# Kernel tuning notes

Hardware: AMD Instinct MI355X
Metric: run time of the kernel (lower is better)

## Reference

```python
import jax, jax.numpy as jnp
import numpy as np

B, T, C, F = 2, 2048, 2048, 8192
LN_EPS = 1e-5


def setup_inputs() -> dict:
    key = jax.random.key(0)
    ks = jax.random.split(key, 24)
    rn = lambda k, s, sc=1.0: jax.random.normal(k, s, jnp.float32) * sc
    un = lambda k, s: jax.random.uniform(k, s, jnp.float32)
    inp = {}
    inp['x'] = rn(ks[0], (B, T, C))
    inp['att_shift'] = rn(ks[1], (B, C))
    # wkv_state rows: aa (num), bb (den), pp (running max exponent)
    inp['wkv_state'] = jnp.stack([jnp.zeros((B, C)), jnp.zeros((B, C)),
                                  jnp.full((B, C), -1e38)], axis=1)
    inp['ffn_shift'] = rn(ks[2], (B, C))
    inp['ln1_g'] = jnp.ones(C); inp['ln1_b'] = jnp.zeros(C)
    inp['ln2_g'] = jnp.ones(C); inp['ln2_b'] = jnp.zeros(C)
    inp['tmk'] = un(ks[3], (C,)); inp['tmv'] = un(ks[4], (C,)); inp['tmr'] = un(ks[5], (C,))
    inp['time_decay'] = rn(ks[6], (C,), 0.5)
    inp['time_first'] = rn(ks[7], (C,), 0.5)
    inp['Wk'] = rn(ks[8], (C, C), 0.02); inp['Wv'] = rn(ks[9], (C, C), 0.02)
    inp['Wr'] = rn(ks[10], (C, C), 0.02); inp['Wo'] = rn(ks[11], (C, C), 0.02)
    inp['fmk'] = un(ks[12], (C,)); inp['fmr'] = un(ks[13], (C,))
    inp['Fk'] = rn(ks[14], (C, F), 0.02)
    inp['Fr'] = rn(ks[15], (C, C), 0.02)
    inp['Fv'] = rn(ks[16], (F, C), 0.02)
    return inp


def layer_norm(x, g, b):
    m = jnp.mean(x, axis=-1, keepdims=True)
    v = jnp.mean(jnp.square(x - m), axis=-1, keepdims=True)
    return (x - m) * jax.lax.rsqrt(v + LN_EPS) * g + b


def wkv(w, u, k, v, state):
    # w: -exp(time_decay) [C], u: time_first [C]; k,v: [B,T,C]; state: [B,3,C]
    def step(carry, kv_t):
        aa, bb, pp = carry
        kt, vt = kv_t
        ww = u + kt
        p = jnp.maximum(pp, ww)
        e1 = jnp.exp(pp - p)
        e2 = jnp.exp(ww - p)
        y = (e1 * aa + e2 * vt) / (e1 * bb + e2)
        ww2 = pp + w
        p2 = jnp.maximum(ww2, kt)
        e1b = jnp.exp(ww2 - p2)
        e2b = jnp.exp(kt - p2)
        return (e1b * aa + e2b * vt, e1b * bb + e2b, p2), y
    carry0 = (state[:, 0], state[:, 1], state[:, 2])
    (aa, bb, pp), ys = jax.lax.scan(step, carry0,
                                    (k.transpose(1, 0, 2), v.transpose(1, 0, 2)))
    return ys.transpose(1, 0, 2), jnp.stack([aa, bb, pp], axis=1)


def reference(x, att_shift, wkv_state, ffn_shift, ln1_g, ln1_b, ln2_g, ln2_b,
              tmk, tmv, tmr, time_decay, time_first, Wk, Wv, Wr, Wo,
              fmk, fmr, Fk, Fr, Fv):
    # ---- time-mix (attention) ----
    x1 = layer_norm(x, ln1_g, ln1_b)
    xx = jnp.concatenate([att_shift[:, None, :], x1[:, :-1]], axis=1)
    xk = x1 * tmk + xx * (1.0 - tmk)
    xv = x1 * tmv + xx * (1.0 - tmv)
    xr = x1 * tmr + xx * (1.0 - tmr)
    k = jnp.einsum('btc,cd->btd', xk, Wk)
    v = jnp.einsum('btc,cd->btd', xv, Wv)
    r = jnp.einsum('btc,cd->btd', xr, Wr)
    y, new_wkv = wkv(-jnp.exp(time_decay), time_first, k, v, wkv_state)
    x = x + jnp.einsum('btd,dc->btc', jax.nn.sigmoid(r) * y, Wo)
    # ---- channel-mix (FFN) ----
    x2 = layer_norm(x, ln2_g, ln2_b)
    xx2 = jnp.concatenate([ffn_shift[:, None, :], x2[:, :-1]], axis=1)
    xk2 = x2 * fmk + xx2 * (1.0 - fmk)
    xr2 = x2 * fmr + xx2 * (1.0 - fmr)
    kf = jnp.square(jax.nn.relu(jnp.einsum('btc,cf->btf', xk2, Fk)))
    kv = jnp.einsum('btf,fc->btc', kf, Fv)
    x = x + jax.nn.sigmoid(jnp.einsum('btc,cd->btd', xr2, Fr)) * kv
    return x, x1[:, -1], new_wkv, x2[:, -1]
```

## Files before the change

### kernel.cpp

```cpp
#include <hip/hip_runtime.h>
#include <stdint.h>

#define B_ 2
#define T_ 2048
#define C_ 2048
#define F_ 8192
#define M_ 4096
#define BC_ 4096
#define CHB 16
#define TCH 16
#define LC2 128

typedef __attribute__((ext_vector_type(8))) __bf16 bf16x8;
typedef __attribute__((ext_vector_type(4))) float f32x4;

__device__ __forceinline__ unsigned short f2bf(float f) {
  union { float f; unsigned u; } v; v.f = f;
  unsigned r = v.u + 0x7fffu + ((v.u >> 16) & 1u);
  return (unsigned short)(r >> 16);
}
__device__ __forceinline__ float b2f(unsigned short h) {
  union { unsigned u; float f; } v; v.u = ((unsigned)h) << 16; return v.f;
}

__device__ __forceinline__ void gload16(const void* g, void* l) {
  __builtin_amdgcn_global_load_lds((__attribute__((address_space(1))) void*)g,
                                   (__attribute__((address_space(3))) void*)l,
                                   16, 0, 0);
}

__global__ __launch_bounds__(256) void k_transpose_cast(
    const float* __restrict__ W, unsigned short* __restrict__ WT, int K, int N) {
  __shared__ unsigned short tile[32][33];
  const int n0 = blockIdx.x * 32, k0 = blockIdx.y * 32;
  const int tx = threadIdx.x & 31, ty = threadIdx.x >> 5;
#pragma unroll
  for (int i = 0; i < 4; ++i)
    tile[ty + 8 * i][tx] = f2bf(W[(size_t)(k0 + ty + 8 * i) * N + n0 + tx]);
  __syncthreads();
#pragma unroll
  for (int i = 0; i < 4; ++i)
    WT[(size_t)(n0 + ty + 8 * i) * K + k0 + tx] = tile[tx][ty + 8 * i];
}

__global__ __launch_bounds__(256) void k_layernorm(
    const float* __restrict__ x, const float* __restrict__ g,
    const float* __restrict__ beta, unsigned short* __restrict__ y,
    float* __restrict__ last_out) {
  const int row = blockIdx.x;
  const int t = row & (T_ - 1);
  const int bi = row >> 11;
  const float* xr = x + (size_t)row * C_;
  const int base = threadIdx.x * 8;
  float lv[8];
  {
    float4 a = *(const float4*)(xr + base);
    float4 b = *(const float4*)(xr + base + 4);
    lv[0]=a.x; lv[1]=a.y; lv[2]=a.z; lv[3]=a.w; lv[4]=b.x; lv[5]=b.y; lv[6]=b.z; lv[7]=b.w;
  }
  float s = 0.f, q = 0.f;
#pragma unroll
  for (int j = 0; j < 8; ++j) { s += lv[j]; q += lv[j] * lv[j]; }
#pragma unroll
  for (int o = 32; o > 0; o >>= 1) { s += __shfl_down(s, o); q += __shfl_down(q, o); }
  __shared__ float rs[4], rq[4];
  if ((threadIdx.x & 63) == 0) { rs[threadIdx.x >> 6] = s; rq[threadIdx.x >> 6] = q; }
  __syncthreads();
  s = rs[0] + rs[1] + rs[2] + rs[3];
  q = rq[0] + rq[1] + rq[2] + rq[3];
  const float mean = s * (1.f / C_);
  const float var = q * (1.f / C_) - mean * mean;
  const float inv = 1.f / sqrtf(var + 1e-5f);
  float ov[8];
  unsigned short o8[8];
#pragma unroll
  for (int j = 0; j < 8; ++j) {
    ov[j] = (lv[j] - mean) * inv * g[base + j] + beta[base + j];
    o8[j] = f2bf(ov[j]);
  }
  *(uint4*)(y + (size_t)row * C_ + base) = *(uint4*)o8;
  if (last_out != nullptr && t == T_ - 1) {
    float* lp = last_out + (size_t)bi * C_ + base;
    *(float4*)lp = make_float4(ov[0], ov[1], ov[2], ov[3]);
    *(float4*)(lp + 4) = make_float4(ov[4], ov[5], ov[6], ov[7]);
  }
}

__global__ __launch_bounds__(256) void k_mix3(
    const unsigned short* __restrict__ x1, const float* __restrict__ shift,
    const float* __restrict__ tmk, const float* __restrict__ tmv,
    const float* __restrict__ tmr,
    unsigned short* __restrict__ xk, unsigned short* __restrict__ xv,
    unsigned short* __restrict__ xr) {
  const int row = blockIdx.x;
  const int t = row & (T_ - 1);
  const int bi = row >> 11;
  const int c0 = threadIdx.x * 8;
  const size_t o = (size_t)row * C_ + c0;
  unsigned short cur8[8];
  *(uint4*)cur8 = *(const uint4*)(x1 + o);
  float pv[8];
  if (t == 0) {
    const float* sp = shift + (size_t)bi * C_ + c0;
#pragma unroll
    for (int j = 0; j < 8; ++j) pv[j] = sp[j];
  } else {
    unsigned short p8[8];
    *(uint4*)p8 = *(const uint4*)(x1 + o - C_);
#pragma unroll
    for (int j = 0; j < 8; ++j) pv[j] = b2f(p8[j]);
  }
  unsigned short ok[8], ov[8], orr[8];
#pragma unroll
  for (int j = 0; j < 8; ++j) {
    const float a = b2f(cur8[j]), p = pv[j];
    const float mk = tmk[c0 + j], mv = tmv[c0 + j], mr = tmr[c0 + j];
    ok[j]  = f2bf(a * mk + p * (1.f - mk));
    ov[j]  = f2bf(a * mv + p * (1.f - mv));
    orr[j] = f2bf(a * mr + p * (1.f - mr));
  }
  *(uint4*)(xk + o) = *(uint4*)ok;
  *(uint4*)(xv + o) = *(uint4*)ov;
  *(uint4*)(xr + o) = *(uint4*)orr;
}

__global__ __launch_bounds__(256) void k_mix2(
    const unsigned short* __restrict__ x2, const float* __restrict__ shift,
    const float* __restrict__ fmk, const float* __restrict__ fmr,
    unsigned short* __restrict__ xk2, unsigned short* __restrict__ xr2) {
  const int row = blockIdx.x;
  const int t = row & (T_ - 1);
  const int bi = row >> 11;
  const int c0 = threadIdx.x * 8;
  const size_t o = (size_t)row * C_ + c0;
  unsigned short cur8[8];
  *(uint4*)cur8 = *(const uint4*)(x2 + o);
  float pv[8];
  if (t == 0) {
    const float* sp = shift + (size_t)bi * C_ + c0;
#pragma unroll
    for (int j = 0; j < 8; ++j) pv[j] = sp[j];
  } else {
    unsigned short p8[8];
    *(uint4*)p8 = *(const uint4*)(x2 + o - C_);
#pragma unroll
    for (int j = 0; j < 8; ++j) pv[j] = b2f(p8[j]);
  }
  unsigned short ok[8], orr[8];
#pragma unroll
  for (int j = 0; j < 8; ++j) {
    const float a = b2f(cur8[j]), p = pv[j];
    const float mk = fmk[c0 + j], mr = fmr[c0 + j];
    ok[j]  = f2bf(a * mk + p * (1.f - mk));
    orr[j] = f2bf(a * mr + p * (1.f - mr));
  }
  *(uint4*)(xk2 + o) = *(uint4*)ok;
  *(uint4*)(xr2 + o) = *(uint4*)orr;
}

__global__ __launch_bounds__(256) void k_wkv_blk(
    const float* __restrict__ kk, const float* __restrict__ vv,
    const float* __restrict__ td, const float* __restrict__ tf,
    const float* __restrict__ st, float* __restrict__ y,
    float* __restrict__ out_state) {
  __shared__ float sA[TCH][CHB], sB[TCH][CHB], sP[TCH][CHB];
  const int blk = blockIdx.x;
  const int bi = blk >> 7;
  const int tx = threadIdx.x & 15;
  const int ty = threadIdx.x >> 4;
  const int c = ((blk & 127) * CHB) + tx;
  const float w = -expf(td[c]);
  const float u = tf[c];
  const size_t base = (size_t)bi * T_ * C_ + (size_t)ty * LC2 * C_ + c;
  const float* kp = kk + base;
  const float* vp = vv + base;
  float aa = 0.f, bb = 0.f, pp = -1e38f;
#pragma unroll 8
  for (int i = 0; i < LC2; ++i) {
    const float kt = kp[(size_t)i * C_], vt = vp[(size_t)i * C_];
    const float ww2 = pp + w;
    const float p2 = fmaxf(ww2, kt);
    const float e1b = expf(ww2 - p2), e2b = expf(kt - p2);
    aa = e1b * aa + e2b * vt;
    bb = e1b * bb + e2b;
    pp = p2;
  }
  sA[ty][tx] = aa; sB[ty][tx] = bb; sP[ty][tx] = pp;
  __syncthreads();
  if (ty == 0) {
    const float* s0 = st + (size_t)bi * 3 * C_;
    float ca = s0[c], cb = s0[C_ + c], cp = s0[2 * C_ + c];
    const float wL = w * (float)LC2;
#pragma unroll
    for (int j = 0; j < TCH; ++j) {
      const float a2 = sA[j][tx], b2 = sB[j][tx], p2 = sP[j][tx];
      sA[j][tx] = ca; sB[j][tx] = cb; sP[j][tx] = cp;
      const float pd = cp + wL;
      const float pm = fmaxf(pd, p2);
      const float e1 = expf(pd - pm), e2 = expf(p2 - pm);
      ca = e1 * ca + e2 * a2;
      cb = e1 * cb + e2 * b2;
      cp = pm;
    }
  }
  __syncthreads();
  aa = sA[ty][tx]; bb = sB[ty][tx]; pp = sP[ty][tx];
  float* yp = y + base;
#pragma unroll 4
  for (int i = 0; i < LC2; ++i) {
    const float kt = kp[(size_t)i * C_], vt = vp[(size_t)i * C_];
    const float ww = u + kt;
    const float p = fmaxf(pp, ww);
    const float e1 = expf(pp - p), e2 = expf(ww - p);
    yp[(size_t)i * C_] = (e1 * aa + e2 * vt) / (e1 * bb + e2);
    const float ww2 = pp + w;
    const float p2 = fmaxf(ww2, kt);
    const float e1b = expf(ww2 - p2), e2b = expf(kt - p2);
    aa = e1b * aa + e2b * vt;
    bb = e1b * bb + e2b;
    pp = p2;
  }
  if (ty == TCH - 1) {
    float* ob = out_state + (size_t)bi * 3 * C_;
    ob[c] = aa; ob[C_ + c] = bb; ob[2 * C_ + c] = pp;
  }
}

__global__ __launch_bounds__(256) void k_sry(
    const unsigned short* __restrict__ r, const float* __restrict__ y,
    unsigned short* __restrict__ sry) {
  const int nv = M_ * C_ / 8;
  for (int i = blockIdx.x * 256 + threadIdx.x; i < nv; i += gridDim.x * 256) {
    unsigned short r8[8];
    *(uint4*)r8 = ((const uint4*)r)[i];
    float4 ya = ((const float4*)y)[2 * i], yb = ((const float4*)y)[2 * i + 1];
    const float yv[8] = {ya.x, ya.y, ya.z, ya.w, yb.x, yb.y, yb.z, yb.w};
    unsigned short o8[8];
#pragma unroll
    for (int j = 0; j < 8; ++j) {
      const float s = 1.f / (1.f + expf(-b2f(r8[j])));
      o8[j] = f2bf(s * yv[j]);
    }
    ((uint4*)sry)[i] = *(uint4*)o8;
  }
}

template <int EPI, int SWZ>
__global__ __launch_bounds__(512, 1) void k_gemm8(
    const unsigned short* __restrict__ A, const unsigned short* __restrict__ BT,
    int K, int Nn, void* __restrict__ out,
    const float* __restrict__ aux1, const float* __restrict__ aux2) {
  __shared__ unsigned short lds[73728];
  const int tid = threadIdx.x;
  const int lane = tid & 63;
  const int wid = tid >> 6;
  int mBase, nBase;
  if (SWZ) {
    const int gx = gridDim.x, gy = gridDim.y;
    const int wg = blockIdx.y * gx + blockIdx.x;
    const int per = (gx * gy) >> 3;
    const int p = 31 - __clz(per);
    const int nr = 1 << ((p - 1) >> 1);
    const int mr = per / nr;
    if ((gx % nr) == 0 && (gy % mr) == 0) {
      const int gxr = gx / nr;
      const int xcd = wg & 7, idx = wg >> 3;
      const int rr = xcd / gxr, rc = xcd % gxr;
      mBase = (rr * mr + idx / nr) * 128;
      nBase = (rc * nr + idx % nr) * 256;
    } else {
      int w2 = (wg & 7) * per + (wg >> 3);
      mBase = (w2 / gx) * 128;
      nBase = (w2 % gx) * 256;
    }
  } else {
    mBase = blockIdx.y * 128;
    nBase = blockIdx.x * 256;
  }
  const int wr = (wid >> 2) * 64;
  const int wc = (wid & 3) * 64;
  const int r16 = lane & 15, kq = lane >> 4;
  const int lrow = lane >> 3;
  const int lslot = (lane & 7) ^ lrow;
  const int xsw = r16 & 7;
  f32x4 acc[4][4] = {};

  const unsigned short* gA0 = A  + (size_t)(mBase + 0   + wid * 8 + lrow) * K + lslot * 8;
  const unsigned short* gA1 = A  + (size_t)(mBase + 64  + wid * 8 + lrow) * K + lslot * 8;
  const unsigned short* gB0 = BT + (size_t)(nBase + 0   + wid * 8 + lrow) * K + lslot * 8;
  const unsigned short* gB1 = BT + (size_t)(nBase + 64  + wid * 8 + lrow) * K + lslot * 8;
  const unsigned short* gB2 = BT + (size_t)(nBase + 128 + wid * 8 + lrow) * K + lslot * 8;
  const unsigned short* gB3 = BT + (size_t)(nBase + 192 + wid * 8 + lrow) * K + lslot * 8;
  const int wof = wid * 512;
  int aoff[4][2], boff[4][2];
#pragma unroll
  for (int m = 0; m < 4; ++m)
#pragma unroll
    for (int s = 0; s < 2; ++s)
      aoff[m][s] = (wr + m * 16 + r16) * 64 + (((s * 4 + kq) ^ xsw) * 8);
#pragma unroll
  for (int n = 0; n < 4; ++n)
#pragma unroll
    for (int s = 0; s < 2; ++s)
      boff[n][s] = 8192 + (wc + n * 16 + r16) * 64 + (((s * 4 + kq) ^ xsw) * 8);

  const int nt = K >> 6;
  gload16(gA0, &lds[0 + wof]);
  gload16(gA1, &lds[4096 + wof]);
  gload16(gB0, &lds[8192 + wof]);
  gload16(gB1, &lds[12288 + wof]);
  gload16(gB2, &lds[16384 + wof]);
  gload16(gB3, &lds[20480 + wof]);
  gload16(gA0 + 64, &lds[24576 + 0 + wof]);
  gload16(gA1 + 64, &lds[24576 + 4096 + wof]);
  gload16(gB0 + 64, &lds[24576 + 8192 + wof]);
  gload16(gB1 + 64, &lds[24576 + 12288 + wof]);
  gload16(gB2 + 64, &lds[24576 + 16384 + wof]);
  gload16(gB3 + 64, &lds[24576 + 20480 + wof]);
  asm volatile("s_waitcnt vmcnt(6)" ::: "memory");
  asm volatile("s_barrier" ::: "memory");

  int cb = 0;
  for (int t = 0; t < nt; ++t) {
    const int nb = (cb >= 1) ? cb - 1 : 2;
    const int ca = cb * 24576;
    const int nba = nb * 24576;
    const int kb2 = (t + 2) << 6;
    const bool pf = (t + 2) < nt;
    if (pf) {
      gload16(gA0 + kb2, &lds[nba + 0 + wof]);
      gload16(gA1 + kb2, &lds[nba + 4096 + wof]);
      gload16(gB0 + kb2, &lds[nba + 8192 + wof]);
      gload16(gB1 + kb2, &lds[nba + 12288 + wof]);
      gload16(gB2 + kb2, &lds[nba + 16384 + wof]);
      gload16(gB3 + kb2, &lds[nba + 20480 + wof]);
    }
    bf16x8 af[4][2], bq[4][2];
#pragma unroll
    for (int m = 0; m < 4; ++m)
#pragma unroll
      for (int s = 0; s < 2; ++s)
        af[m][s] = *(const bf16x8*)&lds[ca + aoff[m][s]];
#pragma unroll
    for (int n = 0; n < 4; ++n)
#pragma unroll
      for (int s = 0; s < 2; ++s)
        bq[n][s] = *(const bf16x8*)&lds[ca + boff[n][s]];
    __builtin_amdgcn_s_setprio(1);
#pragma unroll
    for (int m = 0; m < 4; ++m)
#pragma unroll
      for (int n = 0; n < 4; ++n)
#pragma unroll
        for (int s = 0; s < 2; ++s)
          acc[m][n] = __builtin_amdgcn_mfma_f32_16x16x32_bf16(
              af[m][s], bq[n][s], acc[m][n], 0, 0, 0);
    __builtin_amdgcn_s_setprio(0);
    if (pf) {
      asm volatile("s_waitcnt vmcnt(6)" ::: "memory");
    } else if (t + 1 < nt) {
      asm volatile("s_waitcnt vmcnt(0)" ::: "memory");
    }
    asm volatile("s_barrier" ::: "memory");
    cb = (cb == 2) ? 0 : cb + 1;
  }

  const int c0 = kq * 4;
#pragma unroll
  for (int m = 0; m < 4; ++m) {
#pragma unroll
    for (int n = 0; n < 4; ++n) {
      const int col = nBase + wc + n * 16 + r16;
#pragma unroll
      for (int e = 0; e < 4; ++e) {
        const int rowg = mBase + wr + m * 16 + c0 + e;
        const size_t idx = (size_t)rowg * Nn + col;
        const float va = acc[m][n][e];
        if (EPI == 0) {
          ((float*)out)[idx] = va;
        } else if (EPI == 1) {
          const float t = va > 0.f ? va : 0.f;
          ((unsigned short*)out)[idx] = f2bf(t * t);
        } else if (EPI == 2) {
          ((float*)out)[idx] = aux1[idx] + va;
        } else if (EPI == 3) {
          const float s = 1.f / (1.f + expf(-va));
          ((float*)out)[idx] = aux1[idx] + s * aux2[idx];
        } else {
          ((unsigned short*)out)[idx] = f2bf(va);
        }
      }
    }
  }
}

template <int EPI, int SWZ>
__global__ __launch_bounds__(512, 1) void k_gemm256(
    const unsigned short* __restrict__ A, const unsigned short* __restrict__ BT,
    int K, int Nn, void* __restrict__ out,
    const float* __restrict__ aux1, const float* __restrict__ aux2) {
  __shared__ unsigned short lds[65536];
  const int tid = threadIdx.x;
  const int lane = tid & 63;
  const int wid = tid >> 6;
  int mBase, nBase;
  if (SWZ) {
    const int gx = gridDim.x, gy = gridDim.y;
    const int wg = blockIdx.y * gx + blockIdx.x;
    const int per = (gx * gy) >> 3;
    const int p = 31 - __clz(per);
    const int nr = 1 << (p >> 1);
    const int mr = per / nr;
    if ((gx % nr) == 0 && (gy % mr) == 0) {
      const int gxr = gx / nr;
      const int xcd = wg & 7, idx = wg >> 3;
      const int rr = xcd / gxr, rc = xcd % gxr;
      mBase = (rr * mr + idx / nr) * 256;
      nBase = (rc * nr + idx % nr) * 256;
    } else {
      int w2 = (wg & 7) * per + (wg >> 3);
      mBase = (w2 / gx) * 256;
      nBase = (w2 % gx) * 256;
    }
  } else {
    mBase = blockIdx.y * 256;
    nBase = blockIdx.x * 256;
  }
  const int wr = (wid >> 2) * 128;
  const int wc = (wid & 3) * 64;
  const int r16 = lane & 15, kq = lane >> 4;
  const int lrow = lane >> 3;
  const int lslot = (lane & 7) ^ lrow;
  const int xsw = r16 & 7;
  f32x4 acc[8][4] = {};

  const unsigned short* gA[4];
  const unsigned short* gB[4];
#pragma unroll
  for (int j = 0; j < 4; ++j) {
    gA[j] = A  + (size_t)(mBase + j * 64 + wid * 8 + lrow) * K + lslot * 8;
    gB[j] = BT + (size_t)(nBase + j * 64 + wid * 8 + lrow) * K + lslot * 8;
  }
  const int wof = wid * 512;

  const int nt = K >> 6;
#pragma unroll
  for (int j = 0; j < 4; ++j) {
    gload16(gA[j], &lds[j * 4096 + wof]);
    gload16(gB[j], &lds[16384 + j * 4096 + wof]);
  }
  asm volatile("s_waitcnt vmcnt(0)" ::: "memory");
  asm volatile("s_barrier" ::: "memory");

  for (int t = 0; t < nt; ++t) {
    const int ca = (t & 1) * 32768;
    const int nba = ((t + 1) & 1) * 32768;
    const int kb1 = (t + 1) << 6;
    const bool pf = (t + 1) < nt;
    if (pf) {
#pragma unroll
      for (int j = 0; j < 4; ++j) {
        gload16(gA[j] + kb1, &lds[nba + j * 4096 + wof]);
        gload16(gB[j] + kb1, &lds[nba + 16384 + j * 4096 + wof]);
      }
    }
    bf16x8 bq[4][2];
#pragma unroll
    for (int n = 0; n < 4; ++n)
#pragma unroll
      for (int s = 0; s < 2; ++s)
        bq[n][s] = *(const bf16x8*)&lds[ca + 16384 + (wc + n * 16 + r16) * 64 +
                                        (((s * 4 + kq) ^ xsw) * 8)];
#pragma unroll
    for (int qm = 0; qm < 2; ++qm) {
      bf16x8 af[4][2];
#pragma unroll
      for (int m = 0; m < 4; ++m)
#pragma unroll
        for (int s = 0; s < 2; ++s)
          af[m][s] = *(const bf16x8*)&lds[ca + (wr + (qm * 4 + m) * 16 + r16) * 64 +
                                          (((s * 4 + kq) ^ xsw) * 8)];
      __builtin_amdgcn_s_setprio(1);
#pragma unroll
      for (int m = 0; m < 4; ++m)
#pragma unroll
        for (int n = 0; n < 4; ++n)
#pragma unroll
          for (int s = 0; s < 2; ++s)
            acc[qm * 4 + m][n] = __builtin_amdgcn_mfma_f32_16x16x32_bf16(
                af[m][s], bq[n][s], acc[qm * 4 + m][n], 0, 0, 0);
      __builtin_amdgcn_s_setprio(0);
    }
    if (pf) asm volatile("s_waitcnt vmcnt(0)" ::: "memory");
    asm volatile("s_barrier" ::: "memory");
  }

  const int c0 = kq * 4;
#pragma unroll
  for (int m = 0; m < 8; ++m) {
#pragma unroll
    for (int n = 0; n < 4; ++n) {
      const int col = nBase + wc + n * 16 + r16;
#pragma unroll
      for (int e = 0; e < 4; ++e) {
        const int rowg = mBase + wr + m * 16 + c0 + e;
        const size_t idx = (size_t)rowg * Nn + col;
        const float va = acc[m][n][e];
        if (EPI == 0) {
          ((float*)out)[idx] = va;
        } else if (EPI == 1) {
          const float t = va > 0.f ? va : 0.f;
          ((unsigned short*)out)[idx] = f2bf(t * t);
        } else if (EPI == 2) {
          ((float*)out)[idx] = aux1[idx] + va;
        } else if (EPI == 3) {
          const float s = 1.f / (1.f + expf(-va));
          ((float*)out)[idx] = aux1[idx] + s * aux2[idx];
        } else {
          ((unsigned short*)out)[idx] = f2bf(va);
        }
      }
    }
  }
}

extern "C" void kernel_launch(void* const* d_in, const int* in_sizes, int n_in,
                              void* d_out, int out_size, void* d_ws, size_t ws_size,
                              hipStream_t stream) {
  const float* x          = (const float*)d_in[0];
  const float* att_shift  = (const float*)d_in[1];
  const float* wkv_state  = (const float*)d_in[2];
  const float* ffn_shift  = (const float*)d_in[3];
  const float* ln1_g = (const float*)d_in[4];
  const float* ln1_b = (const float*)d_in[5];
  const float* ln2_g = (const float*)d_in[6];
  const float* ln2_b = (const float*)d_in[7];
  const float* tmk = (const float*)d_in[8];
  const float* tmv = (const float*)d_in[9];
  const float* tmr = (const float*)d_in[10];
  const float* time_decay = (const float*)d_in[11];
  const float* time_first = (const float*)d_in[12];
  const float* Wk = (const float*)d_in[13];
  const float* Wv = (const float*)d_in[14];
  const float* Wr = (const float*)d_in[15];
  const float* Wo = (const float*)d_in[16];
  const float* fmk = (const float*)d_in[17];
  const float* fmr = (const float*)d_in[18];
  const float* Fk = (const float*)d_in[19];
  const float* Fr = (const float*)d_in[20];
  const float* Fv = (const float*)d_in[21];

  const size_t MB = 1ull << 20;
  char* ws = (char*)d_ws;
  if (ws_size < 176 * MB) return;

  unsigned short* Wslot = (unsigned short*)(ws);
  float*          kBuf  = (float*)(ws + 32 * MB);
  float*          vBuf  = (float*)(ws + 64 * MB);
  float*          yBuf  = (float*)(ws + 96 * MB);
  unsigned short* h1    = (unsigned short*)(ws + 128 * MB);
  unsigned short* h2    = (unsigned short*)(ws + 144 * MB);
  unsigned short* h3    = (unsigned short*)(ws + 160 * MB);
  unsigned short* xrT   = (unsigned short*)kBuf;
  unsigned short* kf    = (unsigned short*)kBuf;
  float*          kv    = (float*)h1;

  float* outb    = (float*)d_out;
  float* x1_last = outb + (size_t)M_ * C_;
  float* wkv_out = x1_last + (size_t)B_ * C_;
  float* x2_last = wkv_out + (size_t)B_ * 3 * C_;

  const dim3 gCC(C_ / 32, C_ / 32);
  const dim3 gC8(C_ / 256, M_ / 128);
  const dim3 gF256(F_ / 256, M_ / 256);

  k_layernorm<<<M_, 256, 0, stream>>>(x, ln1_g, ln1_b, h1, x1_last);
  k_mix3<<<M_, 256, 0, stream>>>(h1, att_shift, tmk, tmv, tmr, h2, h3, xrT);
  k_transpose_cast<<<gCC, 256, 0, stream>>>(Wr, Wslot, C_, C_);
  k_gemm8<4,1><<<gC8, 512, 0, stream>>>(xrT, Wslot, C_, C_, h1, nullptr, nullptr);
  k_transpose_cast<<<gCC, 256, 0, stream>>>(Wk, Wslot, C_, C_);
  k_gemm8<0,1><<<gC8, 512, 0, stream>>>(h2, Wslot, C_, C_, kBuf, nullptr, nullptr);
  k_transpose_cast<<<gCC, 256, 0, stream>>>(Wv, Wslot, C_, C_);
  k_gemm8<0,1><<<gC8, 512, 0, stream>>>(h3, Wslot, C_, C_, vBuf, nullptr, nullptr);
  k_wkv_blk<<<dim3(BC_ / CHB), 256, 0, stream>>>(kBuf, vBuf, time_decay, time_first,
                                                 wkv_state, yBuf, wkv_out);
  k_sry<<<1024, 256, 0, stream>>>(h1, yBuf, h2);
  k_transpose_cast<<<gCC, 256, 0, stream>>>(Wo, Wslot, C_, C_);
  k_gemm8<2,1><<<gC8, 512, 0, stream>>>(h2, Wslot, C_, C_, yBuf, x, nullptr);

  k_layernorm<<<M_, 256, 0, stream>>>(yBuf, ln2_g, ln2_b, h1, x2_last);
  k_mix2<<<M_, 256, 0, stream>>>(h1, ffn_shift, fmk, fmr, h2, h3);
  k_transpose_cast<<<dim3(F_ / 32, C_ / 32), 256, 0, stream>>>(Fk, Wslot, C_, F_);
  k_gemm256<1,1><<<gF256, 512, 0, stream>>>(h2, Wslot, C_, F_, kf, nullptr, nullptr);
  k_transpose_cast<<<dim3(C_ / 32, F_ / 32), 256, 0, stream>>>(Fv, Wslot, F_, C_);
  k_gemm8<0,1><<<gC8, 512, 0, stream>>>(kf, Wslot, F_, C_, kv, nullptr, nullptr);
  k_transpose_cast<<<gCC, 256, 0, stream>>>(Fr, Wslot, C_, C_);
  k_gemm8<3,1><<<gC8, 512, 0, stream>>>(h3, Wslot, C_, C_, d_out, yBuf, kv);
}
```

Measured before the change: 644.2 us.

## Fuse sigmoid(r)*y into WKV scan and batch attention weight transposes

The separate sigmoid(r)*y pass is folded into the second loop of the WKV scan, which now writes bf16 sr*y directly instead of an fp32 y buffer. This removes one full-size fp32 write and read plus a kernel launch. The four attention weight transposes are merged into one launch that runs up front, writing into four distinct slots of the weight workspace. The transpose tile is widened to 64x32 with packed 32-bit stores. The WKV kernel gains extra strided bf16 loads of r and a sigmoid per element inside its sequential loop.

```diff
diff --git a/kernel.cpp b/kernel.cpp
--- a/kernel.cpp
+++ b/kernel.cpp
@@ -29,18 +29,36 @@
                                    16, 0, 0);
 }
 
-__global__ __launch_bounds__(256) void k_transpose_cast(
+__device__ __forceinline__ void transpose_tile(
+    const float* __restrict__ W, unsigned short* __restrict__ out,
+    int K, int N, int k0, int n0) {
+  __shared__ unsigned short tile[32][66];
+  const int tx = threadIdx.x & 31, ty = threadIdx.x >> 5;
+#pragma unroll
+  for (int i = 0; i < 8; ++i)
+    tile[tx][ty + 8 * i] = f2bf(W[(size_t)(k0 + ty + 8 * i) * N + n0 + tx]);
+  __syncthreads();
+#pragma unroll
+  for (int j = 0; j < 4; ++j) {
+    const int nn = ty + 8 * j;
+    const unsigned pk = *(const unsigned*)&tile[nn][2 * tx];
+    *(unsigned*)&out[(size_t)(n0 + nn) * K + k0 + 2 * tx] = pk;
+  }
+}
+
+__global__ __launch_bounds__(256) void k_transpose4(
+    const float* __restrict__ W0, const float* __restrict__ W1,
+    const float* __restrict__ W2, const float* __restrict__ W3,
+    unsigned short* __restrict__ WT) {
+  const float* W = (blockIdx.z == 0) ? W0 : (blockIdx.z == 1) ? W1
+                   : (blockIdx.z == 2) ? W2 : W3;
+  unsigned short* out = WT + (size_t)blockIdx.z * C_ * C_;
+  transpose_tile(W, out, C_, C_, blockIdx.x * 64, blockIdx.y * 32);
+}
+
+__global__ __launch_bounds__(256) void k_transpose1(
     const float* __restrict__ W, unsigned short* __restrict__ WT, int K, int N) {
-  __shared__ unsigned short tile[32][33];
-  const int n0 = blockIdx.x * 32, k0 = blockIdx.y * 32;
-  const int tx = threadIdx.x & 31, ty = threadIdx.x >> 5;
-#pragma unroll
-  for (int i = 0; i < 4; ++i)
-    tile[ty + 8 * i][tx] = f2bf(W[(size_t)(k0 + ty + 8 * i) * N + n0 + tx]);
-  __syncthreads();
-#pragma unroll
-  for (int i = 0; i < 4; ++i)
-    WT[(size_t)(n0 + ty + 8 * i) * K + k0 + tx] = tile[tx][ty + 8 * i];
+  transpose_tile(W, WT, K, N, blockIdx.x * 64, blockIdx.y * 32);
 }
 
 __global__ __launch_bounds__(256) void k_layernorm(
@@ -158,10 +176,11 @@
   *(uint4*)(xr2 + o) = *(uint4*)orr;
 }
 
-__global__ __launch_bounds__(256) void k_wkv_blk(
+__global__ __launch_bounds__(256) void k_wkv_sry(
     const float* __restrict__ kk, const float* __restrict__ vv,
+    const unsigned short* __restrict__ rr,
     const float* __restrict__ td, const float* __restrict__ tf,
-    const float* __restrict__ st, float* __restrict__ y,
+    const float* __restrict__ st, unsigned short* __restrict__ sry,
     float* __restrict__ out_state) {
   __shared__ float sA[TCH][CHB], sB[TCH][CHB], sP[TCH][CHB];
   const int blk = blockIdx.x;
@@ -205,14 +224,18 @@
   }
   __syncthreads();
   aa = sA[ty][tx]; bb = sB[ty][tx]; pp = sP[ty][tx];
-  float* yp = y + base;
+  const unsigned short* rp = rr + base;
+  unsigned short* sp2 = sry + base;
 #pragma unroll 4
   for (int i = 0; i < LC2; ++i) {
     const float kt = kp[(size_t)i * C_], vt = vp[(size_t)i * C_];
     const float ww = u + kt;
     const float p = fmaxf(pp, ww);
     const float e1 = expf(pp - p), e2 = expf(ww - p);
-    yp[(size_t)i * C_] = (e1 * aa + e2 * vt) / (e1 * bb + e2);
+    const float yv = (e1 * aa + e2 * vt) / (e1 * bb + e2);
+    const float rv = b2f(rp[(size_t)i * C_]);
+    const float sg = 1.f / (1.f + expf(-rv));
+    sp2[(size_t)i * C_] = f2bf(sg * yv);
     const float ww2 = pp + w;
     const float p2 = fmaxf(ww2, kt);
     const float e1b = expf(ww2 - p2), e2b = expf(kt - p2);
@@ -223,25 +246,6 @@
   if (ty == TCH - 1) {
     float* ob = out_state + (size_t)bi * 3 * C_;
     ob[c] = aa; ob[C_ + c] = bb; ob[2 * C_ + c] = pp;
-  }
-}
-
-__global__ __launch_bounds__(256) void k_sry(
-    const unsigned short* __restrict__ r, const float* __restrict__ y,
-    unsigned short* __restrict__ sry) {
-  const int nv = M_ * C_ / 8;
-  for (int i = blockIdx.x * 256 + threadIdx.x; i < nv; i += gridDim.x * 256) {
-    unsigned short r8[8];
-    *(uint4*)r8 = ((const uint4*)r)[i];
-    float4 ya = ((const float4*)y)[2 * i], yb = ((const float4*)y)[2 * i + 1];
-    const float yv[8] = {ya.x, ya.y, ya.z, ya.w, yb.x, yb.y, yb.z, yb.w};
-    unsigned short o8[8];
-#pragma unroll
-    for (int j = 0; j < 8; ++j) {
-      const float s = 1.f / (1.f + expf(-b2f(r8[j])));
-      o8[j] = f2bf(s * yv[j]);
-    }
-    ((uint4*)sry)[i] = *(uint4*)o8;
   }
 }
 
@@ -564,36 +568,35 @@
   unsigned short* xrT   = (unsigned short*)kBuf;
   unsigned short* kf    = (unsigned short*)kBuf;
   float*          kv    = (float*)h1;
+  unsigned short* sWr = Wslot + 0 * (size_t)C_ * C_;
+  unsigned short* sWk = Wslot + 1 * (size_t)C_ * C_;
+  unsigned short* sWv = Wslot + 2 * (size_t)C_ * C_;
+  unsigned short* sWo = Wslot + 3 * (size_t)C_ * C_;
 
   float* outb    = (float*)d_out;
   float* x1_last = outb + (size_t)M_ * C_;
   float* wkv_out = x1_last + (size_t)B_ * C_;
   float* x2_last = wkv_out + (size_t)B_ * 3 * C_;
 
-  const dim3 gCC(C_ / 32, C_ / 32);
   const dim3 gC8(C_ / 256, M_ / 128);
   const dim3 gF256(F_ / 256, M_ / 256);
 
+  k_transpose4<<<dim3(C_ / 64, C_ / 32, 4), 256, 0, stream>>>(Wr, Wk, Wv, Wo, Wslot);
   k_layernorm<<<M_, 256, 0, stream>>>(x, ln1_g, ln1_b, h1, x1_last);
   k_mix3<<<M_, 256, 0, stream>>>(h1, att_shift, tmk, tmv, tmr, h2, h3, xrT);
-  k_transpose_cast<<<gCC, 256, 0, stream>>>(Wr, Wslot, C_, C_);
-  k_gemm8<4,1><<<gC8, 512, 0, stream>>>(xrT, Wslot, C_, C_, h1, nullptr, nullptr);
-  k_transpose_cast<<<gCC, 256, 0, stream>>>(Wk, Wslot, C_, C_);
-  k_gemm8<0,1><<<gC8, 512, 0, stream>>>(h2, Wslot, C_, C_, kBuf, nullptr, nullptr);
-  k_transpose_cast<<<gCC, 256, 0, stream>>>(Wv, Wslot, C_, C_);
-  k_gemm8<0,1><<<gC8, 512, 0, stream>>>(h3, Wslot, C_, C_, vBuf, nullptr, nullptr);
-  k_wkv_blk<<<dim3(BC_ / CHB), 256, 0, stream>>>(kBuf, vBuf, time_decay, time_first,
-                                                 wkv_state, yBuf, wkv_out);
-  k_sry<<<1024, 256, 0, stream>>>(h1, yBuf, h2);
-  k_transpose_cast<<<gCC, 256, 0, stream>>>(Wo, Wslot, C_, C_);
-  k_gemm8<2,1><<<gC8, 512, 0, stream>>>(h2, Wslot, C_, C_, yBuf, x, nullptr);
+  k_gemm8<4,1><<<gC8, 512, 0, stream>>>(xrT, sWr, C_, C_, h1, nullptr, nullptr);
+  k_gemm8<0,1><<<gC8, 512, 0, stream>>>(h2, sWk, C_, C_, kBuf, nullptr, nullptr);
+  k_gemm8<0,1><<<gC8, 512, 0, stream>>>(h3, sWv, C_, C_, vBuf, nullptr, nullptr);
+  k_wkv_sry<<<dim3(BC_ / CHB), 256, 0, stream>>>(kBuf, vBuf, h1, time_decay, time_first,
+                                                 wkv_state, h2, wkv_out);
+  k_gemm8<2,1><<<gC8, 512, 0, stream>>>(h2, sWo, C_, C_, yBuf, x, nullptr);
 
   k_layernorm<<<M_, 256, 0, stream>>>(yBuf, ln2_g, ln2_b, h1, x2_last);
   k_mix2<<<M_, 256, 0, stream>>>(h1, ffn_shift, fmk, fmr, h2, h3);
-  k_transpose_cast<<<dim3(F_ / 32, C_ / 32), 256, 0, stream>>>(Fk, Wslot, C_, F_);
+  k_transpose1<<<dim3(C_ / 64, F_ / 32), 256, 0, stream>>>(Fk, Wslot, C_, F_);
   k_gemm256<1,1><<<gF256, 512, 0, stream>>>(h2, Wslot, C_, F_, kf, nullptr, nullptr);
-  k_transpose_cast<<<dim3(C_ / 32, F_ / 32), 256, 0, stream>>>(Fv, Wslot, F_, C_);
+  k_transpose1<<<dim3(F_ / 64, C_ / 32), 256, 0, stream>>>(Fv, Wslot, F_, C_);
   k_gemm8<0,1><<<gC8, 512, 0, stream>>>(kf, Wslot, F_, C_, kv, nullptr, nullptr);
-  k_transpose_cast<<<gCC, 256, 0, stream>>>(Fr, Wslot, C_, C_);
+  k_transpose1<<<dim3(C_ / 64, C_ / 32), 256, 0, stream>>>(Fr, Wslot, C_, C_);
   k_gemm8<3,1><<<gC8, 512, 0, stream>>>(h3, Wslot, C_, C_, d_out, yBuf, kv);
 }
```

Result: faster. 629.4 us (-2.3%).
